# Optimization experiments

Hardware: AMD Instinct MI355X
Metric: run time of the kernel (lower is better)

## Reference

```python
import jax, jax.numpy as jnp
import numpy as np
from jax.scipy.special import logsumexp

B, S, E, H = 32, 1024, 512, 256  # batch, seq_len, sent_emb_dim, per-direction lstm hidden
NT, NTB = 16, 5
PAD, SOS, EOS = 0, 1, 2
NEG = -1000000.0


def _lstm(x, h0, c0, wih, whh, bih, bhh):
    # x: [B,S,I] -> outputs [B,S,H]; torch gate order i,f,g,o
    def step(carry, xt):
        h, c = carry
        z = xt @ wih.T + h @ whh.T + bih + bhh
        i, f, g, o = jnp.split(z, 4, axis=-1)
        c = jax.nn.sigmoid(f) * c + jax.nn.sigmoid(i) * jnp.tanh(g)
        h = jax.nn.sigmoid(o) * jnp.tanh(c)
        return (h, c), h
    _, hs = jax.lax.scan(step, (h0, c0), jnp.swapaxes(x, 0, 1))
    return jnp.swapaxes(hs, 0, 1)


def _bilstm(x, h0, c0, pf, pb):
    fwd = _lstm(x, h0[0], c0[0], *pf)
    bwd = _lstm(x[:, ::-1], h0[1], c0[1], *pb)[:, ::-1]
    return jnp.concatenate([fwd, bwd], axis=-1)  # [B,S,2H]


def _crf_nll(emissions, tags, mask, T):
    # gold-path score
    first = T[SOS, tags[:, 0]] + jnp.take_along_axis(emissions[:, 0], tags[:, 0:1], axis=1)[:, 0]
    e = jnp.take_along_axis(emissions, tags[:, :, None], axis=2)[:, :, 0]        # [B,S]
    tr = T[tags[:, :-1], tags[:, 1:]]                                            # [B,S-1]
    scores = first + jnp.sum((e[:, 1:] + tr) * mask[:, 1:], axis=1)
    last_idx = mask.sum(1).astype(jnp.int32) - 1
    last_tags = jnp.take_along_axis(tags, last_idx[:, None], axis=1)[:, 0]
    scores = scores + T[last_tags, EOS]
    # log partition via sequential DP (scan over time)
    alphas0 = T[SOS][None, :] + emissions[:, 0]
    es = jnp.swapaxes(emissions, 0, 1)[1:]   # [S-1,B,nt]
    ms = mask.T[1:]                          # [S-1,B]
    def step(alphas, inp):
        e_t, m_t = inp
        sc = e_t[:, None, :] + T[None, :, :] + alphas[:, :, None]  # [B,nt,nt]
        new = logsumexp(sc, axis=1)
        m = m_t[:, None]
        return m * new + (1.0 - m) * alphas, None
    alphas, _ = jax.lax.scan(step, alphas0, (es, ms))
    logZ = logsumexp(alphas + T[:, EOS][None, :], axis=1)
    return -jnp.sum(scores - logZ)


def _make_trans(key, nt):
    t = jax.random.uniform(key, (nt, nt), minval=-0.1, maxval=0.1)
    t = t.at[:, SOS].set(NEG).at[EOS, :].set(NEG)
    t = t.at[PAD, :].set(NEG).at[:, PAD].set(NEG)
    t = t.at[PAD, EOS].set(0.0).at[PAD, PAD].set(0.0)
    return t


def setup_inputs() -> dict:
    key = jax.random.key(0)
    ks = iter(jax.random.split(key, 40))
    sc = 0.05
    inp = {}
    inp['x'] = jax.random.normal(next(ks), (B, S, E), jnp.float32)
    inp['x_binary'] = jax.random.normal(next(ks), (B, S, 3 * E), jnp.float32)
    lengths = jax.random.randint(next(ks), (B,), S // 2, S + 1)
    inp['mask'] = (jnp.arange(S)[None, :] < lengths[:, None]).astype(jnp.float32)
    tg = jax.random.randint(next(ks), (B, S), 3, NT)
    inp['tags'] = jnp.where(inp['mask'] > 0, tg, PAD).astype(jnp.int32)
    tgb = jax.random.randint(next(ks), (B, S), 3, NTB)
    inp['tags_bin'] = jnp.where(inp['mask'] > 0, tgb, PAD).astype(jnp.int32)
    inp['trans'] = _make_trans(next(ks), NT)
    inp['trans_bin'] = _make_trans(next(ks), NTB)
    # binary emitter BiLSTM (input 3E)
    for nm, shp in [('w2f_ih', (4 * H, 3 * E)), ('w2f_hh', (4 * H, H)), ('b2f_ih', (4 * H,)), ('b2f_hh', (4 * H,)),
                    ('w2b_ih', (4 * H, 3 * E)), ('w2b_hh', (4 * H, H)), ('b2b_ih', (4 * H,)), ('b2b_hh', (4 * H,)),
                    ('w_bin', (NTB, 2 * H)), ('bb_bin', (NTB,)),
                    ('w1f_ih', (4 * H, E)), ('w1f_hh', (4 * H, H)), ('b1f_ih', (4 * H,)), ('b1f_hh', (4 * H,)),
                    ('w1b_ih', (4 * H, E)), ('w1b_hh', (4 * H, H)), ('b1b_ih', (4 * H,)), ('b1b_hh', (4 * H,)),
                    ('w_tag', (NT, 4 * H)), ('b_tag', (NT,))]:
        inp[nm] = jax.random.normal(next(ks), shp, jnp.float32) * sc
    inp['h0_bin'] = jax.random.normal(next(ks), (2, B, H), jnp.float32)
    inp['c0_bin'] = jax.random.normal(next(ks), (2, B, H), jnp.float32)
    inp['h0_main'] = jax.random.normal(next(ks), (2, B, H), jnp.float32)
    inp['c0_main'] = jax.random.normal(next(ks), (2, B, H), jnp.float32)
    return inp


def reference(x, x_binary, mask, tags, tags_bin, trans, trans_bin,
              w2f_ih, w2f_hh, b2f_ih, b2f_hh, w2b_ih, w2b_hh, b2b_ih, b2b_hh, w_bin, bb_bin, h0_bin, c0_bin,
              w1f_ih, w1f_hh, b1f_ih, b1f_hh, w1b_ih, w1b_hh, b1b_ih, b1b_hh, w_tag, b_tag, h0_main, c0_main):
    # binary branch: BiLSTM over 3E features -> hidden [B,S,2H] and 5-tag emissions
    hid_bin = _bilstm(x_binary, h0_bin, c0_bin,
                      (w2f_ih, w2f_hh, b2f_ih, b2f_hh), (w2b_ih, w2b_hh, b2b_ih, b2b_hh))
    emis_bin = hid_bin @ w_bin.T + bb_bin
    # main branch: BiLSTM over E features, concat with binary hidden -> n_tags emissions
    hid_main = _bilstm(x, h0_main, c0_main,
                       (w1f_ih, w1f_hh, b1f_ih, b1f_hh), (w1b_ih, w1b_hh, b1b_ih, b1b_hh))
    final = jnp.concatenate([hid_main, hid_bin], axis=-1)  # [B,S,4H] (dropout omitted: eval mode)
    emis = final @ w_tag.T + b_tag
    nll = _crf_nll(emis, tags, mask, trans)
    nll_bin = _crf_nll(emis_bin, tags_bin, mask, trans_bin)
    return jnp.stack([nll, nll_bin])
```

## Files before the change

### kernel.cpp

```cpp
#include <hip/hip_runtime.h>

typedef _Float16 f16;
typedef _Float16 f16x2 __attribute__((ext_vector_type(2)));
typedef _Float16 f16x4 __attribute__((ext_vector_type(4)));
typedef _Float16 f16x8 __attribute__((ext_vector_type(8)));
typedef float f32x4 __attribute__((ext_vector_type(4)));
typedef int iv4 __attribute__((ext_vector_type(4)));

#define S_LEN 1024
#define BATCH 32
#define HID 256
#define L2E 1.4426950408889634f
#define L2E2 2.8853900817779268f

#if __has_builtin(__builtin_amdgcn_fdot2)
#define FDOT2(a, b, c) __builtin_amdgcn_fdot2((a), (b), (c), false)
#else
static __device__ __forceinline__ float FDOT2(f16x2 a, f16x2 b, float c) {
  return c + (float)a[0] * (float)b[0] + (float)a[1] * (float)b[1];
}
#endif

__device__ __forceinline__ float EXP2(float x) {
#if __has_builtin(__builtin_amdgcn_exp2f)
  return __builtin_amdgcn_exp2f(x);
#else
  return exp2f(x);
#endif
}
__device__ __forceinline__ float RCP(float x) {
#if __has_builtin(__builtin_amdgcn_rcpf)
  return __builtin_amdgcn_rcpf(x);
#else
  return 1.0f / x;
#endif
}

__device__ __forceinline__ iv4 cvt8(float4 a, float4 b) {
#if __has_builtin(__builtin_amdgcn_cvt_pkrtz)
  auto p0 = __builtin_amdgcn_cvt_pkrtz(a.x, a.y);
  auto p1 = __builtin_amdgcn_cvt_pkrtz(a.z, a.w);
  auto p2 = __builtin_amdgcn_cvt_pkrtz(b.x, b.y);
  auto p3 = __builtin_amdgcn_cvt_pkrtz(b.z, b.w);
  iv4 o;
  o[0] = __builtin_bit_cast(int, p0);
  o[1] = __builtin_bit_cast(int, p1);
  o[2] = __builtin_bit_cast(int, p2);
  o[3] = __builtin_bit_cast(int, p3);
  return o;
#else
  f16x8 h;
  h[0] = (f16)a.x; h[1] = (f16)a.y; h[2] = (f16)a.z; h[3] = (f16)a.w;
  h[4] = (f16)b.x; h[5] = (f16)b.y; h[6] = (f16)b.z; h[7] = (f16)b.w;
  return __builtin_bit_cast(iv4, h);
#endif
}

#if __has_builtin(__builtin_amdgcn_global_load_lds)
__device__ __forceinline__ void gload16(const void* g, void* l) {
  __builtin_amdgcn_global_load_lds((const __attribute__((address_space(1))) void*)g,
                                   (__attribute__((address_space(3))) void*)l, 16, 0, 0);
}
#else
__device__ __forceinline__ void gload16(const void* g, void* l) {
  int lane = __builtin_amdgcn_mbcnt_hi(~0u, __builtin_amdgcn_mbcnt_lo(~0u, 0));
  ((f16x8*)l)[lane] = *(const f16x8*)g;
}
#endif

#define WG_BARRIER()                                                  \
  do {                                                                \
    __builtin_amdgcn_sched_barrier(0);                                \
    asm volatile("s_waitcnt lgkmcnt(0)\n\ts_barrier" ::: "memory");   \
    __builtin_amdgcn_sched_barrier(0);                                \
  } while (0)

__device__ __forceinline__ float dot8(f16x8 w, f16x8 h, float acc) {
  f16x2 a, b;
  a[0] = w[0]; a[1] = w[1]; b[0] = h[0]; b[1] = h[1]; acc = FDOT2(a, b, acc);
  a[0] = w[2]; a[1] = w[3]; b[0] = h[2]; b[1] = h[3]; acc = FDOT2(a, b, acc);
  a[0] = w[4]; a[1] = w[5]; b[0] = h[4]; b[1] = h[5]; acc = FDOT2(a, b, acc);
  a[0] = w[6]; a[1] = w[7]; b[0] = h[6]; b[1] = h[7]; acc = FDOT2(a, b, acc);
  return acc;
}

__global__ __launch_bounds__(256) void prep_all(
    const float* __restrict__ w1f_hh, const float* __restrict__ w1b_hh,
    const float* __restrict__ w2f_hh, const float* __restrict__ w2b_hh,
    char* __restrict__ Wq4, float* __restrict__ fsc4,
    const float* __restrict__ w_tag, f16* __restrict__ wtag,
    const float* __restrict__ w_bin, f16* __restrict__ wbin,
    const float* __restrict__ w1f_ih, const float* __restrict__ w1b_ih,
    const float* __restrict__ w2f_ih, const float* __restrict__ w2b_ih,
    f16* __restrict__ w16all,
    const float* __restrict__ b1f_ih, const float* __restrict__ b1f_hh,
    const float* __restrict__ b1b_ih, const float* __restrict__ b1b_hh,
    const float* __restrict__ b2f_ih, const float* __restrict__ b2f_hh,
    const float* __restrict__ b2b_ih, const float* __restrict__ b2b_hh,
    float* __restrict__ bsum) {
  const int blk = blockIdx.x;
  const int tid = threadIdx.x;
  if (blk < 1024) {
    const int u = blk >> 8, sb = blk & 255;
    const float* src = u == 0 ? w1f_hh : u == 1 ? w1b_hh : u == 2 ? w2f_hh : w2b_hh;
    char* dstq = Wq4 + (size_t)u * 262144;
    float* fsc = fsc4 + u * 1024;
    const int row = sb * 4 + (tid >> 6);
    const int lane = tid & 63;
    const float sc = (row >= 512 && row < 768) ? L2E2 : L2E;
    float4 v = *(const float4*)(src + (size_t)row * 256 + lane * 4);
    float w0 = v.x * sc, w1 = v.y * sc, w2 = v.z * sc, w3 = v.w * sc;
    float mx = fmaxf(fmaxf(fabsf(w0), fabsf(w1)), fmaxf(fabsf(w2), fabsf(w3)));
#pragma unroll
    for (int off = 1; off < 64; off <<= 1) mx = fmaxf(mx, __shfl_xor(mx, off));
    mx = fmaxf(mx, 1e-20f);
    float inv = 127.0f / mx;
    int q0 = (int)rintf(w0 * inv), q1 = (int)rintf(w1 * inv);
    int q2 = (int)rintf(w2 * inv), q3 = (int)rintf(w3 * inv);
    int pk = (q0 & 0xff) | ((q1 & 0xff) << 8) | ((q2 & 0xff) << 16) | ((q3 & 0xff) << 24);
    ((int*)(dstq + (size_t)row * 256))[lane] = pk;
    if (lane == 0) fsc[row] = mx / 16129.0f;
  } else if (blk < 1040) {
    int i = (blk - 1024) * 256 + tid;
    if (i < 4096) {
      float4 v = ((const float4*)w_tag)[i];
      f16x4 h;
      h[0] = (f16)v.x; h[1] = (f16)v.y; h[2] = (f16)v.z; h[3] = (f16)v.w;
      ((f16x4*)wtag)[i] = h;
    }
  } else if (blk < 1043) {
    int i = (blk - 1040) * 256 + tid;
    if (i < 640) {
      float4 v = ((const float4*)w_bin)[i];
      f16x4 h;
      h[0] = (f16)v.x; h[1] = (f16)v.y; h[2] = (f16)v.z; h[3] = (f16)v.w;
      ((f16x4*)wbin)[i] = h;
    }
  } else if (blk < 3091) {
    int rel = blk - 1043;
    const float* src;
    f16* dst;
    int K, total8;
    if (rel < 256) { src = w1f_ih; dst = w16all; K = 512; total8 = 65536; }
    else if (rel < 512) { src = w1b_ih; dst = w16all + 524288; K = 512; total8 = 65536; rel -= 256; }
    else if (rel < 1280) { src = w2f_ih; dst = w16all + 1048576; K = 1536; total8 = 196608; rel -= 512; }
    else { src = w2b_ih; dst = w16all + 2621440; K = 1536; total8 = 196608; rel -= 1280; }
    int i = rel * 256 + tid;
    if (i < total8) {
      int row = (int)(((long long)i * 8) / K);
      float sc = (row >= 512 && row < 768) ? L2E2 : L2E;
      const float* s = src + (size_t)i * 8;
      float4 a = *(const float4*)s;
      float4 b = *(const float4*)(s + 4);
      f16x8 h;
      h[0] = (f16)(a.x * sc); h[1] = (f16)(a.y * sc); h[2] = (f16)(a.z * sc); h[3] = (f16)(a.w * sc);
      h[4] = (f16)(b.x * sc); h[5] = (f16)(b.y * sc); h[6] = (f16)(b.z * sc); h[7] = (f16)(b.w * sc);
      *(f16x8*)(dst + (size_t)i * 8) = h;
    }
  } else {
    int i = (blk - 3091) * 256 + tid;
    if (i < 4096) {
      int u = i >> 10, n = i & 1023;
      float sc = (n >= 512 && n < 768) ? L2E2 : L2E;
      const float* pa = u == 0 ? b1f_ih : u == 1 ? b1b_ih : u == 2 ? b2f_ih : b2b_ih;
      const float* ph = u == 0 ? b1f_hh : u == 1 ? b1b_hh : u == 2 ? b2f_hh : b2b_hh;
      bsum[i] = (pa[n] + ph[n]) * sc;
    }
  }
}

__global__ __launch_bounds__(256) void proj_gemm(const float* __restrict__ x,
                                                 const float* __restrict__ xbin,
                                                 const f16* __restrict__ w16all,
                                                 const float* __restrict__ bsum,
                                                 char* __restrict__ P4) {
  __shared__ __align__(16) char smem[98304];
  const int L = blockIdx.x;
  const int xcd = L & 7;
  const int k = L >> 3;
  const int e = k & 7;
  const int G = xcd + ((k >> 3) << 3);
  const int v = e >> 1;
  const int ubit = e & 1;
  const int pair = G >> 8;
  const int bm = G & 255;
  const int unit = pair * 2 + ubit;
  const int K = (pair == 0) ? 512 : 1536;
  const float* Aptr = (pair == 0) ? x : xbin;
  const size_t woff = (unit == 0) ? 0u : (unit == 1) ? 524288u : (unit == 2) ? 1048576u : 2621440u;
  const f16* W16 = w16all + woff;
  const int bgrp = bm >> 5, t0 = (bm & 31) * 32;
  const int b0 = bgrp * 4, c = bgrp >> 1, lkb = bgrp & 1;
  const int tid = threadIdx.x;
  const int lane = tid & 63, wid = tid >> 6;
  const int wm = wid >> 1, wn = wid & 1;
  const int lr = lane & 15, lk = lane >> 4;
  const int xsw = (lr & 7) << 4;

  f32x4 acc[4][8];
#pragma unroll
  for (int i = 0; i < 4; ++i)
#pragma unroll
    for (int n = 0; n < 8; ++n) acc[i][n] = (f32x4){0.f, 0.f, 0.f, 0.f};

#define PROJ_PREFETCH(KN_, AO_, BO_)                                                        \
  if ((KN_) < K) {                                                                          \
    float4 ar0[4], ar1[4];                                                                  \
    _Pragma("unroll") for (int s = 0; s < 4; ++s) {                                         \
      int slot = s * 256 + tid;                                                             \
      int row = slot >> 3, seg = slot & 7;                                                  \
      size_t arow = (size_t)(b0 + (row >> 5)) * 1024 + t0 + (row & 31);                     \
      const float* ga = Aptr + arow * K + (KN_) + seg * 8;                                  \
      ar0[s] = *(const float4*)ga;                                                          \
      ar1[s] = *(const float4*)(ga + 4);                                                    \
    }                                                                                       \
    __builtin_amdgcn_sched_barrier(0);                                                      \
    _Pragma("unroll") for (int i = 0; i < 8; ++i) {                                         \
      int g = (wid * 8 + i) * 64 + lane;                                                    \
      int brow = g >> 3, cg = g & 7;                                                        \
      const f16* bsrc = W16 + (size_t)(v * 256 + brow) * K + (KN_) + ((cg ^ (brow & 7)) << 3); \
      gload16(bsrc, smem + (BO_) + (wid * 8 + i) * 1024);                                   \
    }                                                                                       \
    __builtin_amdgcn_sched_barrier(0);                                                      \
    _Pragma("unroll") for (int s = 0; s < 4; ++s) {                                         \
      int slot = s * 256 + tid;                                                             \
      int row = slot >> 3, seg = slot & 7;                                                  \
      *(iv4*)(smem + (AO_) + row * 128 + ((seg ^ (row & 7)) << 4)) = cvt8(ar0[s], ar1[s]);  \
    }                                                                                       \
    __builtin_amdgcn_sched_barrier(0);                                                      \
  } else {                                                                                  \
    __builtin_amdgcn_sched_barrier(0);                                                      \
    asm volatile("s_waitcnt vmcnt(0)" ::: "memory");                                        \
    __builtin_amdgcn_sched_barrier(0);                                                      \
  }

#define PROJ_COMPUTE(AO_, BO_)                                                              \
  _Pragma("unroll") for (int kk = 0; kk < 2; ++kk) {                                        \
    f16x8 af[4], bf[8];                                                                     \
    _Pragma("unroll") for (int mi = 0; mi < 4; ++mi) {                                      \
      int ba = (wm * 64 + mi * 16 + lr) * 128 + kk * 64 + lk * 16;                          \
      af[mi] = *(const f16x8*)(smem + (AO_) + (ba ^ xsw));                                  \
    }                                                                                       \
    _Pragma("unroll") for (int ni = 0; ni < 8; ++ni) {                                      \
      int bb = (wn * 128 + ni * 16 + lr) * 128 + kk * 64 + lk * 16;                         \
      bf[ni] = *(const f16x8*)(smem + (BO_) + (bb ^ xsw));                                  \
    }                                                                                       \
    _Pragma("unroll") for (int mi = 0; mi < 4; ++mi)                                        \
      _Pragma("unroll") for (int ni = 0; ni < 8; ++ni)                                      \
        acc[mi][ni] = __builtin_amdgcn_mfma_f32_16x16x32_f16(af[mi], bf[ni], acc[mi][ni], 0, 0, 0); \
  }

  PROJ_PREFETCH(0, 0, 32768);
  for (int k0 = 0; k0 < K; k0 += 128) {
    PROJ_PREFETCH(k0 + 64, 16384, 65536);
    WG_BARRIER();
    PROJ_COMPUTE(0, 32768);
    WG_BARRIER();
    PROJ_PREFETCH(k0 + 128, 0, 32768);
    WG_BARRIER();
    PROJ_COMPUTE(16384, 65536);
    WG_BARRIER();
  }
#undef PROJ_PREFETCH
#undef PROJ_COMPUTE

  float biasv[8];
#pragma unroll
  for (int ni = 0; ni < 8; ++ni)
    biasv[ni] = bsum[unit * 1024 + v * 256 + wn * 128 + ni * 16 + lr];
  char* Pv = P4 + ((size_t)unit << 26) + ((size_t)v << 24);
#pragma unroll
  for (int pass = 0; pass < 2; ++pass) {
    __syncthreads();
#pragma unroll
    for (int mi2 = 0; mi2 < 2; ++mi2) {
      int mi = mi2 * 2 + pass;
#pragma unroll
      for (int ni = 0; ni < 8; ++ni) {
        int col = wn * 128 + ni * 16 + lr;
        int wc = col >> 5, jc = (col >> 4) & 1, lc = col & 15;
#pragma unroll
        for (int rr = 0; rr < 4; ++rr) {
          int row = wm * 64 + mi * 16 + lk * 4 + rr;
          int bsub = row >> 5, tl = row & 15;
          int unit2 = tl * 256 + wc * 32 + jc * 16 + lc;
          int off = (unit2 * 8 + bsub * 2) ^ ((tl & 7) << 4);
          *(f16*)(smem + off) = (f16)(acc[mi][ni][rr] + biasv[ni]);
        }
      }
    }
    __syncthreads();
#pragma unroll
    for (int kq = 0; kq < 16; ++kq) {
      int uid = kq * 256 + tid;
      int tl = uid >> 8, sub = uid & 255;
      int off = (uid * 8) ^ ((tl & 7) << 4);
      unsigned long long val = *(const unsigned long long*)(smem + off);
      int t_loc = pass * 16 + tl;
      int wq = sub >> 5, jq = (sub >> 4) & 1, lq = sub & 15;
      size_t didx =
          (((size_t)((t0 + t_loc) * 4 + c) * 512) + wq * 64 + jq * 32 + lkb * 16 + lq) << 3;
      *(unsigned long long*)(Pv + didx) = val;
    }
  }
}

__global__ __attribute__((amdgpu_flat_work_group_size(512, 512), amdgpu_waves_per_eu(2, 2)))
void lstm_rec5(const char* __restrict__ Wq4,
               const float* __restrict__ fsc4,
               const char* __restrict__ P4,
               const float* __restrict__ h0m,
               const float* __restrict__ c0m,
               const float* __restrict__ h0b,
               const float* __restrict__ c0b,
               f16* __restrict__ hid4) {
  const int wg = blockIdx.x;
  const int u = wg >> 4, c16 = wg & 15;
  const int dir = u & 1;
  const int tid = threadIdx.x;
  const int l = tid & 63, w = tid >> 6;
  const int lr = l & 15, lk = l >> 4;
  const int jj = lk >> 1, selb = lk & 1;
  const int r2 = lr & 1;
  const int swzA = r2 ? 80 : 0;
  const int swzW = selb ? 80 : 0;
  const int j = w * 32 + jj * 16 + lr;

  __shared__ __align__(16) char hbuf[2][512];

  iv4 Bf[4][8];
  const char* wb = Wq4 + ((size_t)u << 18);
#pragma unroll
  for (int nt = 0; nt < 8; ++nt) {
    int n = (nt >> 1) * 256 + w * 32 + ((nt & 1) << 4) + lr;
#pragma unroll
    for (int ks = 0; ks < 4; ++ks)
      Bf[ks][nt] = *(const iv4*)(wb + (size_t)n * 256 + ks * 64 + lk * 16);
  }
  float fv[4], fv4[4];
#pragma unroll
  for (int v = 0; v < 4; ++v) {
    fv[v] = fsc4[u * 1024 + v * 256 + j];
    fv4[v] = fv[v] * 4.f;
  }

  const int b = c16 * 2 + selb;
  const float* h0 = (u < 2 ? h0m : h0b) + (size_t)dir * BATCH * HID;
  const float* c0 = (u < 2 ? c0m : c0b) + (size_t)dir * BATCH * HID;
  float cst = c0[b * HID + j];
  {
    float hv = h0[b * HID + j] * 31.75f;
    int hq = (int)rintf(hv);
    hq = hq > 127 ? 127 : (hq < -127 ? -127 : hq);
    hbuf[0][selb * 256 + (j ^ swzW)] = (char)hq;
  }

  const char* Pc = P4 + ((size_t)u << 26);
  const size_t soff =
      (size_t)((w * 64 + jj * 32 + (((c16 >> 1) & 1) << 4) + lr) * 8 + (c16 & 1) * 4);
  const int cq = c16 >> 2;
  f16x2 Pa[4], Pb[4];
  {
    int t0 = dir ? (S_LEN - 1) : 0;
    size_t tb = ((size_t)((t0 << 2) + cq) << 12) + soff;
#pragma unroll
    for (int v = 0; v < 4; ++v) Pa[v] = *(const f16x2*)(Pc + ((size_t)v << 24) + tb);
  }
  WG_BARRIER();

#define LSTM_STEP(S_, SP_, PC_, PN_, FV_)                                                   \
  {                                                                                         \
    const int t = dir ? (S_LEN - 1 - (S_)) : (S_);                                          \
    {                                                                                       \
      int s2 = ((S_) + 1 < S_LEN) ? (S_) + 1 : (S_);                                        \
      int t2 = dir ? (S_LEN - 1 - s2) : s2;                                                 \
      size_t tb = ((size_t)((t2 << 2) + cq) << 12) + soff;                                  \
      _Pragma("unroll") for (int v = 0; v < 4; ++v)                                         \
          PN_[v] = *(const f16x2*)(Pc + ((size_t)v << 24) + tb);                            \
    }                                                                                       \
    iv4 ia[8];                                                                              \
    _Pragma("unroll") for (int nt = 0; nt < 8; ++nt) ia[nt] = (iv4){0, 0, 0, 0};            \
    const char* hb = hbuf[SP_];                                                             \
    _Pragma("unroll") for (int ks = 0; ks < 4; ++ks) {                                      \
      iv4 Af = *(const iv4*)(hb + r2 * 256 + ((ks * 64 + lk * 16) ^ swzA));                 \
      _Pragma("unroll") for (int nt = 0; nt < 8; ++nt)                                      \
          ia[nt] = __builtin_amdgcn_mfma_i32_16x16x64_i8(Af, Bf[ks][nt], ia[nt], 0, 0, 0);  \
    }                                                                                       \
    float z[4];                                                                             \
    _Pragma("unroll") for (int v = 0; v < 4; ++v) {                                         \
      int e0 = selb ? ia[v * 2][1] : ia[v * 2][0];                                          \
      int e1 = selb ? ia[v * 2 + 1][1] : ia[v * 2 + 1][0];                                  \
      int iz = jj ? e1 : e0;                                                                \
      float pv = selb ? (float)PC_[v][1] : (float)PC_[v][0];                                \
      z[v] = pv + FV_[v] * (float)iz;                                                       \
    }                                                                                       \
    float zi = z[0], zf = z[1], zg = z[2], zo = z[3];                                       \
    float ei = EXP2(-zi), ef = EXP2(-zf), eg = EXP2(-zg), eo = EXP2(-zo);                   \
    float di = 1.f + ei, df = 1.f + ef, dg = 1.f + eg, dof = 1.f + eo;                      \
    float r1 = RCP(di * df);                                                                \
    float si = r1 * df, sf = r1 * di;                                                       \
    float r2x = RCP(dg * dof);                                                              \
    float tg = 2.f * (r2x * dof) - 1.f, so = r2x * dg;                                      \
    float cc = sf * cst + si * tg;                                                          \
    cst = cc;                                                                               \
    float ec = EXP2(-L2E2 * cc);                                                            \
    float th = 2.f * RCP(1.f + ec) - 1.f;                                                   \
    float hh = so * th;                                                                     \
    int hq = (int)rintf(hh * 127.f);                                                        \
    hbuf[SP_ ^ 1][selb * 256 + (j ^ swzW)] = (char)hq;                                      \
    hid4[((size_t)b << 20) + ((size_t)t << 10) + (u << 8) + j] = (f16)hh;                   \
    WG_BARRIER();                                                                           \
  }

  LSTM_STEP(0, 0, Pa, Pb, fv4);
  for (int s = 1; s <= 1021; s += 2) {
    LSTM_STEP(s, 1, Pb, Pa, fv);
    LSTM_STEP(s + 1, 0, Pa, Pb, fv);
  }
  LSTM_STEP(1023, 1, Pb, Pa, fv);
#undef LSTM_STEP
}

__global__ __launch_bounds__(256) void emis_mfma(const f16* __restrict__ hid4,
                                                 const f16* __restrict__ wtag,
                                                 const float* __restrict__ btag,
                                                 const f16* __restrict__ wbin,
                                                 const float* __restrict__ bbin,
                                                 float* __restrict__ emis,
                                                 float* __restrict__ emisb) {
  __shared__ __align__(16) f16 wt[16 * 1024];
  __shared__ __align__(16) f16 wbp[16 * 512];
  const int tid = threadIdx.x;
#pragma unroll
  for (int i = 0; i < 8; ++i) {
    int idx = i * 256 + tid;
    int n = idx >> 7, cc = idx & 127;
    ((f16x8*)wt)[n * 128 + (cc ^ (n & 7))] = ((const f16x8*)wtag)[idx];
  }
#pragma unroll
  for (int i = 0; i < 4; ++i) {
    int idx = i * 256 + tid;
    int n = idx >> 6, cc = idx & 63;
    f16x8 val = {};
    if (n < 5) val = ((const f16x8*)wbin)[n * 64 + cc];
    ((f16x8*)wbp)[n * 64 + (cc ^ (n & 7))] = val;
  }
  __syncthreads();

  const int wv = tid >> 6, lane = tid & 63;
  const int lr = lane & 15, lk = lane >> 4;
  const size_t row0 = (size_t)blockIdx.x * 64 + wv * 16;
  const f16* arow = hid4 + (row0 + lr) * 1024;
  const f16x8* wtp = (const f16x8*)wt;
  const f16x8* wbv = (const f16x8*)wbp;
  const int bsw = lr & 7;

  f32x4 accm = (f32x4){0.f, 0.f, 0.f, 0.f};
  f32x4 accb = (f32x4){0.f, 0.f, 0.f, 0.f};
#pragma unroll
  for (int ks = 0; ks < 32; ++ks) {
    f16x8 a = *(const f16x8*)(arow + ks * 32 + lk * 8);
    f16x8 b = wtp[lr * 128 + ((ks * 4 + lk) ^ bsw)];
    accm = __builtin_amdgcn_mfma_f32_16x16x32_f16(a, b, accm, 0, 0, 0);
  }
#pragma unroll
  for (int ks = 0; ks < 16; ++ks) {
    f16x8 a = *(const f16x8*)(arow + 512 + ks * 32 + lk * 8);
    f16x8 b = wbv[lr * 64 + ((ks * 4 + lk) ^ bsw)];
    accb = __builtin_amdgcn_mfma_f32_16x16x32_f16(a, b, accb, 0, 0, 0);
  }
  float bt = btag[lr];
  float bb = (lr < 5) ? bbin[lr] : 0.f;
#pragma unroll
  for (int r = 0; r < 4; ++r) {
    size_t orow = row0 + lk * 4 + r;
    emis[orow * 16 + lr] = accm[r] + bt;
    if (lr < 5) emisb[orow * 5 + lr] = accb[r] + bb;
  }
}

__global__ __launch_bounds__(64) void crf_fused(const float* __restrict__ emis,
                                                const float* __restrict__ trans,
                                                const float* __restrict__ emisb,
                                                const float* __restrict__ transb,
                                                const float* __restrict__ mask,
                                                const int* __restrict__ tags,
                                                const int* __restrict__ tagsb,
                                                float* __restrict__ outLogZ,
                                                float* __restrict__ outScore) {
  const int lane = threadIdx.x;
  if (blockIdx.x < 64) {
    const int crf = blockIdx.x >> 5, b = blockIdx.x & 31;
    const int NTc = crf ? 5 : 16;
    const float* __restrict__ E = crf ? emisb : emis;
    const float* __restrict__ T = crf ? transb : trans;
    const int jn = lane >> 2, p = lane & 3;
    const bool jv = (jn < NTc);
    const int jc = jv ? jn : 0;
    float Tc[4];
#pragma unroll
    for (int ii = 0; ii < 4; ++ii) {
      int i = p * 4 + ii;
      Tc[ii] = (jv && i < NTc) ? T[i * NTc + jn] : -1e30f;
    }
    float alpha = jv ? (T[1 * NTc + jc] + E[(size_t)(b << 10) * NTc + jc]) : -1e30f;
    const size_t ebase = (size_t)(b << 10) * NTc + jc;
    const int mbase = b << 10;
#define LDE(tt) E[ebase + (size_t)(tt)*NTc]
#define LDM(tt) mask[mbase + (tt)]

    auto step = [&](float e_tj, float m_t) {
      float a0 = __shfl(alpha, ((p * 4 + 0) << 2) | p);
      float a1 = __shfl(alpha, ((p * 4 + 1) << 2) | p);
      float a2 = __shfl(alpha, ((p * 4 + 2) << 2) | p);
      float a3 = __shfl(alpha, ((p * 4 + 3) << 2) | p);
      float v0 = a0 + Tc[0], v1 = a1 + Tc[1], v2 = a2 + Tc[2], v3 = a3 + Tc[3];
      float mx = fmaxf(fmaxf(v0, v1), fmaxf(v2, v3));
      mx = fmaxf(mx, __shfl_xor(mx, 1, 4));
      mx = fmaxf(mx, __shfl_xor(mx, 2, 4));
      float ss = __expf(v0 - mx) + __expf(v1 - mx) + __expf(v2 - mx) + __expf(v3 - mx);
      ss += __shfl_xor(ss, 1, 4);
      ss += __shfl_xor(ss, 2, 4);
      float newv = e_tj + mx + __logf(ss);
      alpha = (m_t > 0.5f) ? newv : alpha;
    };

    float eb[4], mb[4];
#pragma unroll
    for (int k = 0; k < 4; ++k) { eb[k] = LDE(1 + k); mb[k] = LDM(1 + k); }
    for (int t = 1; t <= 1017; t += 4) {
      float en[4], mn[4];
#pragma unroll
      for (int k = 0; k < 4; ++k) {
        int ix = t + 4 + k;
        ix = ix > 1023 ? 1023 : ix;
        en[k] = LDE(ix);
        mn[k] = LDM(ix);
      }
      step(eb[0], mb[0]); step(eb[1], mb[1]); step(eb[2], mb[2]); step(eb[3], mb[3]);
#pragma unroll
      for (int k = 0; k < 4; ++k) { eb[k] = en[k]; mb[k] = mn[k]; }
    }
    step(eb[0], mb[0]); step(eb[1], mb[1]); step(eb[2], mb[2]);
#undef LDE
#undef LDM

    float fin = (jv && p == 0) ? (alpha + T[jn * NTc + 2]) : -1e30f;
    float mx = fin;
#pragma unroll
    for (int off = 1; off < 64; off <<= 1) mx = fmaxf(mx, __shfl_xor(mx, off));
    float ss = __expf(fin - mx);
#pragma unroll
    for (int off = 1; off < 64; off <<= 1) ss += __shfl_xor(ss, off);
    if (lane == 0) outLogZ[crf * 32 + b] = mx + __logf(ss);
  } else {
    const int bi = blockIdx.x - 64;
    const int crf = bi >> 5, b = bi & 31;
    const int NTc = crf ? 5 : 16;
    const float* __restrict__ E = crf ? emisb : emis;
    const float* __restrict__ T = crf ? transb : trans;
    const int* __restrict__ tg = (crf ? tagsb : tags) + (b << 10);
    const float* __restrict__ mk = mask + (b << 10);
    float s = 0.f, cnt = 0.f;
    for (int t = lane; t < S_LEN; t += 64) {
      float m = mk[t];
      cnt += m;
      if (t >= 1 && m > 0.5f)
        s += E[((size_t)(b << 10) + t) * NTc + tg[t]] + T[tg[t - 1] * NTc + tg[t]];
    }
#pragma unroll
    for (int off = 32; off >= 1; off >>= 1) {
      s += __shfl_down(s, off);
      cnt += __shfl_down(cnt, off);
    }
    if (lane == 0) {
      int L = (int)(cnt + 0.5f);
      int t0 = tg[0];
      float tot = T[1 * NTc + t0] + E[(size_t)(b << 10) * NTc + t0] + s + T[tg[L - 1] * NTc + 2];
      outScore[crf * 32 + b] = tot;
    }
  }
}

__global__ void finalk(const float* __restrict__ logZ, const float* __restrict__ score,
                       float* __restrict__ out) {
  int j = threadIdx.x;
  if (j < 2) {
    float a = 0.f;
    for (int b = 0; b < 32; ++b) a += logZ[j * 32 + b] - score[j * 32 + b];
    out[j] = a;
  }
}

extern "C" void kernel_launch(void* const* d_in, const int* in_sizes, int n_in,
                              void* d_out, int out_size, void* d_ws, size_t ws_size,
                              hipStream_t stream) {
  const float* x       = (const float*)d_in[0];
  const float* xbin    = (const float*)d_in[1];
  const float* mask    = (const float*)d_in[2];
  const int*   tags    = (const int*)d_in[3];
  const int*   tagsb   = (const int*)d_in[4];
  const float* trans   = (const float*)d_in[5];
  const float* transb  = (const float*)d_in[6];
  const float* w2f_ih  = (const float*)d_in[7];
  const float* w2f_hh  = (const float*)d_in[8];
  const float* b2f_ih  = (const float*)d_in[9];
  const float* b2f_hh  = (const float*)d_in[10];
  const float* w2b_ih  = (const float*)d_in[11];
  const float* w2b_hh  = (const float*)d_in[12];
  const float* b2b_ih  = (const float*)d_in[13];
  const float* b2b_hh  = (const float*)d_in[14];
  const float* w_bin   = (const float*)d_in[15];
  const float* bb_bin  = (const float*)d_in[16];
  const float* w1f_ih  = (const float*)d_in[17];
  const float* w1f_hh  = (const float*)d_in[18];
  const float* b1f_ih  = (const float*)d_in[19];
  const float* b1f_hh  = (const float*)d_in[20];
  const float* w1b_ih  = (const float*)d_in[21];
  const float* w1b_hh  = (const float*)d_in[22];
  const float* b1b_ih  = (const float*)d_in[23];
  const float* b1b_hh  = (const float*)d_in[24];
  const float* w_tag   = (const float*)d_in[25];
  const float* b_tag   = (const float*)d_in[26];
  const float* h0_bin  = (const float*)d_in[27];
  const float* c0_bin  = (const float*)d_in[28];
  const float* h0_main = (const float*)d_in[29];
  const float* c0_main = (const float*)d_in[30];

  char* ws = (char*)d_ws;
  char* P4    = ws;
  f16* hid4   = (f16*)(ws + 268435456);
  char* Wq4   = ws + 335544320;
  float* fsc4 = (float*)(ws + 336592896);
  f16* wtag   = (f16*)(ws + 336609280);
  f16* wbin   = (f16*)(ws + 336642048);
  float* emis  = (float*)(ws + 336647168);
  float* emisb = (float*)(ws + 338744320);
  float* logZ  = (float*)(ws + 339399680);
  float* score = (float*)(ws + 339399936);
  float* bsum  = (float*)(ws + 339400704);
  f16* w16all  = (f16*)(ws + 340000768);

  prep_all<<<3107, 256, 0, stream>>>(w1f_hh, w1b_hh, w2f_hh, w2b_hh, Wq4, fsc4,
                                     w_tag, wtag, w_bin, wbin,
                                     w1f_ih, w1b_ih, w2f_ih, w2b_ih, w16all,
                                     b1f_ih, b1f_hh, b1b_ih, b1b_hh,
                                     b2f_ih, b2f_hh, b2b_ih, b2b_hh, bsum);
  proj_gemm<<<4096, 256, 0, stream>>>(x, xbin, w16all, bsum, P4);
  lstm_rec5<<<64, 512, 0, stream>>>(Wq4, fsc4, P4, h0_main, c0_main, h0_bin, c0_bin, hid4);
  emis_mfma<<<512, 256, 0, stream>>>(hid4, wtag, b_tag, wbin, bb_bin, emis, emisb);
  crf_fused<<<128, 64, 0, stream>>>(emis, trans, emisb, transb, mask, tags, tagsb, logZ, score);
  finalk<<<1, 64, 0, stream>>>(logZ, score, (float*)d_out);
}
```

Measured before the change: 1.606 ms.

## Fuse input projection GEMM and LSTM recurrence with flag-based producer/consumer overlap

Merges the projection GEMM and the recurrent LSTM kernel into one launch. The first 64 blocks run the recurrence, and the remaining blocks compute projection tiles, ordered so that time windows are produced from both ends first. Recurrence blocks spin on per-window atomic flags before reading each 32-step window, so the GEMM can overlap with the serial recurrence instead of running fully before it. The costs are 512-thread blocks where half the threads idle in the GEMM part, lower occupancy for the GEMM blocks, spin-wait overhead, and a deadlock risk if the recurrence blocks are not scheduled alongside the producers.

```diff
diff --git a/kernel.cpp b/kernel.cpp
--- a/kernel.cpp
+++ b/kernel.cpp
@@ -82,6 +82,10 @@
   a[0] = w[4]; a[1] = w[5]; b[0] = h[4]; b[1] = h[5]; acc = FDOT2(a, b, acc);
   a[0] = w[6]; a[1] = w[7]; b[0] = h[6]; b[1] = h[7]; acc = FDOT2(a, b, acc);
   return acc;
+}
+
+__global__ void zerof(unsigned* __restrict__ f) {
+  f[blockIdx.x * 256 + threadIdx.x] = 0u;
 }
 
 __global__ __launch_bounds__(256) void prep_all(
@@ -169,204 +173,83 @@
   }
 }
 
-__global__ __launch_bounds__(256) void proj_gemm(const float* __restrict__ x,
-                                                 const float* __restrict__ xbin,
-                                                 const f16* __restrict__ w16all,
-                                                 const float* __restrict__ bsum,
-                                                 char* __restrict__ P4) {
-  __shared__ __align__(16) char smem[98304];
-  const int L = blockIdx.x;
-  const int xcd = L & 7;
-  const int k = L >> 3;
-  const int e = k & 7;
-  const int G = xcd + ((k >> 3) << 3);
-  const int v = e >> 1;
-  const int ubit = e & 1;
-  const int pair = G >> 8;
-  const int bm = G & 255;
-  const int unit = pair * 2 + ubit;
-  const int K = (pair == 0) ? 512 : 1536;
-  const float* Aptr = (pair == 0) ? x : xbin;
-  const size_t woff = (unit == 0) ? 0u : (unit == 1) ? 524288u : (unit == 2) ? 1048576u : 2621440u;
-  const f16* W16 = w16all + woff;
-  const int bgrp = bm >> 5, t0 = (bm & 31) * 32;
-  const int b0 = bgrp * 4, c = bgrp >> 1, lkb = bgrp & 1;
-  const int tid = threadIdx.x;
-  const int lane = tid & 63, wid = tid >> 6;
-  const int wm = wid >> 1, wn = wid & 1;
-  const int lr = lane & 15, lk = lane >> 4;
-  const int xsw = (lr & 7) << 4;
-
-  f32x4 acc[4][8];
-#pragma unroll
-  for (int i = 0; i < 4; ++i)
-#pragma unroll
-    for (int n = 0; n < 8; ++n) acc[i][n] = (f32x4){0.f, 0.f, 0.f, 0.f};
-
-#define PROJ_PREFETCH(KN_, AO_, BO_)                                                        \
-  if ((KN_) < K) {                                                                          \
-    float4 ar0[4], ar1[4];                                                                  \
-    _Pragma("unroll") for (int s = 0; s < 4; ++s) {                                         \
-      int slot = s * 256 + tid;                                                             \
-      int row = slot >> 3, seg = slot & 7;                                                  \
-      size_t arow = (size_t)(b0 + (row >> 5)) * 1024 + t0 + (row & 31);                     \
-      const float* ga = Aptr + arow * K + (KN_) + seg * 8;                                  \
-      ar0[s] = *(const float4*)ga;                                                          \
-      ar1[s] = *(const float4*)(ga + 4);                                                    \
-    }                                                                                       \
-    __builtin_amdgcn_sched_barrier(0);                                                      \
-    _Pragma("unroll") for (int i = 0; i < 8; ++i) {                                         \
-      int g = (wid * 8 + i) * 64 + lane;                                                    \
-      int brow = g >> 3, cg = g & 7;                                                        \
-      const f16* bsrc = W16 + (size_t)(v * 256 + brow) * K + (KN_) + ((cg ^ (brow & 7)) << 3); \
-      gload16(bsrc, smem + (BO_) + (wid * 8 + i) * 1024);                                   \
-    }                                                                                       \
-    __builtin_amdgcn_sched_barrier(0);                                                      \
-    _Pragma("unroll") for (int s = 0; s < 4; ++s) {                                         \
-      int slot = s * 256 + tid;                                                             \
-      int row = slot >> 3, seg = slot & 7;                                                  \
-      *(iv4*)(smem + (AO_) + row * 128 + ((seg ^ (row & 7)) << 4)) = cvt8(ar0[s], ar1[s]);  \
-    }                                                                                       \
-    __builtin_amdgcn_sched_barrier(0);                                                      \
-  } else {                                                                                  \
-    __builtin_amdgcn_sched_barrier(0);                                                      \
-    asm volatile("s_waitcnt vmcnt(0)" ::: "memory");                                        \
-    __builtin_amdgcn_sched_barrier(0);                                                      \
-  }
-
-#define PROJ_COMPUTE(AO_, BO_)                                                              \
-  _Pragma("unroll") for (int kk = 0; kk < 2; ++kk) {                                        \
-    f16x8 af[4], bf[8];                                                                     \
-    _Pragma("unroll") for (int mi = 0; mi < 4; ++mi) {                                      \
-      int ba = (wm * 64 + mi * 16 + lr) * 128 + kk * 64 + lk * 16;                          \
-      af[mi] = *(const f16x8*)(smem + (AO_) + (ba ^ xsw));                                  \
-    }                                                                                       \
-    _Pragma("unroll") for (int ni = 0; ni < 8; ++ni) {                                      \
-      int bb = (wn * 128 + ni * 16 + lr) * 128 + kk * 64 + lk * 16;                         \
-      bf[ni] = *(const f16x8*)(smem + (BO_) + (bb ^ xsw));                                  \
-    }                                                                                       \
-    _Pragma("unroll") for (int mi = 0; mi < 4; ++mi)                                        \
-      _Pragma("unroll") for (int ni = 0; ni < 8; ++ni)                                      \
-        acc[mi][ni] = __builtin_amdgcn_mfma_f32_16x16x32_f16(af[mi], bf[ni], acc[mi][ni], 0, 0, 0); \
-  }
-
-  PROJ_PREFETCH(0, 0, 32768);
-  for (int k0 = 0; k0 < K; k0 += 128) {
-    PROJ_PREFETCH(k0 + 64, 16384, 65536);
-    WG_BARRIER();
-    PROJ_COMPUTE(0, 32768);
-    WG_BARRIER();
-    PROJ_PREFETCH(k0 + 128, 0, 32768);
-    WG_BARRIER();
-    PROJ_COMPUTE(16384, 65536);
-    WG_BARRIER();
-  }
-#undef PROJ_PREFETCH
-#undef PROJ_COMPUTE
-
-  float biasv[8];
-#pragma unroll
-  for (int ni = 0; ni < 8; ++ni)
-    biasv[ni] = bsum[unit * 1024 + v * 256 + wn * 128 + ni * 16 + lr];
-  char* Pv = P4 + ((size_t)unit << 26) + ((size_t)v << 24);
-#pragma unroll
-  for (int pass = 0; pass < 2; ++pass) {
-    __syncthreads();
-#pragma unroll
-    for (int mi2 = 0; mi2 < 2; ++mi2) {
-      int mi = mi2 * 2 + pass;
-#pragma unroll
-      for (int ni = 0; ni < 8; ++ni) {
-        int col = wn * 128 + ni * 16 + lr;
-        int wc = col >> 5, jc = (col >> 4) & 1, lc = col & 15;
-#pragma unroll
-        for (int rr = 0; rr < 4; ++rr) {
-          int row = wm * 64 + mi * 16 + lk * 4 + rr;
-          int bsub = row >> 5, tl = row & 15;
-          int unit2 = tl * 256 + wc * 32 + jc * 16 + lc;
-          int off = (unit2 * 8 + bsub * 2) ^ ((tl & 7) << 4);
-          *(f16*)(smem + off) = (f16)(acc[mi][ni][rr] + biasv[ni]);
-        }
-      }
-    }
-    __syncthreads();
-#pragma unroll
-    for (int kq = 0; kq < 16; ++kq) {
-      int uid = kq * 256 + tid;
-      int tl = uid >> 8, sub = uid & 255;
-      int off = (uid * 8) ^ ((tl & 7) << 4);
-      unsigned long long val = *(const unsigned long long*)(smem + off);
-      int t_loc = pass * 16 + tl;
-      int wq = sub >> 5, jq = (sub >> 4) & 1, lq = sub & 15;
-      size_t didx =
-          (((size_t)((t0 + t_loc) * 4 + c) * 512) + wq * 64 + jq * 32 + lkb * 16 + lq) << 3;
-      *(unsigned long long*)(Pv + didx) = val;
-    }
-  }
-}
-
 __global__ __attribute__((amdgpu_flat_work_group_size(512, 512), amdgpu_waves_per_eu(2, 2)))
-void lstm_rec5(const char* __restrict__ Wq4,
+void proj_lstm(const float* __restrict__ x,
+               const float* __restrict__ xbin,
+               const f16* __restrict__ w16all,
+               const float* __restrict__ bsum,
+               char* __restrict__ P4,
+               const char* __restrict__ Wq4,
                const float* __restrict__ fsc4,
-               const char* __restrict__ P4,
                const float* __restrict__ h0m,
                const float* __restrict__ c0m,
                const float* __restrict__ h0b,
                const float* __restrict__ c0b,
-               f16* __restrict__ hid4) {
-  const int wg = blockIdx.x;
-  const int u = wg >> 4, c16 = wg & 15;
-  const int dir = u & 1;
+               f16* __restrict__ hid4,
+               unsigned* __restrict__ flags) {
+  __shared__ __align__(16) char smem[98304];
+  __shared__ __align__(16) char hbuf[2][512];
   const int tid = threadIdx.x;
-  const int l = tid & 63, w = tid >> 6;
-  const int lr = l & 15, lk = l >> 4;
-  const int jj = lk >> 1, selb = lk & 1;
-  const int r2 = lr & 1;
-  const int swzA = r2 ? 80 : 0;
-  const int swzW = selb ? 80 : 0;
-  const int j = w * 32 + jj * 16 + lr;
-
-  __shared__ __align__(16) char hbuf[2][512];
-
-  iv4 Bf[4][8];
-  const char* wb = Wq4 + ((size_t)u << 18);
-#pragma unroll
-  for (int nt = 0; nt < 8; ++nt) {
-    int n = (nt >> 1) * 256 + w * 32 + ((nt & 1) << 4) + lr;
-#pragma unroll
-    for (int ks = 0; ks < 4; ++ks)
-      Bf[ks][nt] = *(const iv4*)(wb + (size_t)n * 256 + ks * 64 + lk * 16);
-  }
-  float fv[4], fv4[4];
-#pragma unroll
-  for (int v = 0; v < 4; ++v) {
-    fv[v] = fsc4[u * 1024 + v * 256 + j];
-    fv4[v] = fv[v] * 4.f;
-  }
-
-  const int b = c16 * 2 + selb;
-  const float* h0 = (u < 2 ? h0m : h0b) + (size_t)dir * BATCH * HID;
-  const float* c0 = (u < 2 ? c0m : c0b) + (size_t)dir * BATCH * HID;
-  float cst = c0[b * HID + j];
-  {
-    float hv = h0[b * HID + j] * 31.75f;
-    int hq = (int)rintf(hv);
-    hq = hq > 127 ? 127 : (hq < -127 ? -127 : hq);
-    hbuf[0][selb * 256 + (j ^ swzW)] = (char)hq;
-  }
-
-  const char* Pc = P4 + ((size_t)u << 26);
-  const size_t soff =
-      (size_t)((w * 64 + jj * 32 + (((c16 >> 1) & 1) << 4) + lr) * 8 + (c16 & 1) * 4);
-  const int cq = c16 >> 2;
-  f16x2 Pa[4], Pb[4];
-  {
-    int t0 = dir ? (S_LEN - 1) : 0;
-    size_t tb = ((size_t)((t0 << 2) + cq) << 12) + soff;
-#pragma unroll
-    for (int v = 0; v < 4; ++v) Pa[v] = *(const f16x2*)(Pc + ((size_t)v << 24) + tb);
-  }
-  WG_BARRIER();
+
+  if (blockIdx.x < 64) {
+    const int wg = blockIdx.x;
+    const int u = wg >> 4, c16 = wg & 15;
+    const int dir = u & 1;
+    const int l = tid & 63, w = tid >> 6;
+    const int lr = l & 15, lk = l >> 4;
+    const int jj = lk >> 1, selb = lk & 1;
+    const int r2 = lr & 1;
+    const int swzA = r2 ? 80 : 0;
+    const int swzW = selb ? 80 : 0;
+    const int j = w * 32 + jj * 16 + lr;
+
+    iv4 Bf[4][8];
+    const char* wb = Wq4 + ((size_t)u << 18);
+#pragma unroll
+    for (int nt = 0; nt < 8; ++nt) {
+      int n = (nt >> 1) * 256 + w * 32 + ((nt & 1) << 4) + lr;
+#pragma unroll
+      for (int ks = 0; ks < 4; ++ks)
+        Bf[ks][nt] = *(const iv4*)(wb + (size_t)n * 256 + ks * 64 + lk * 16);
+    }
+    float fv[4], fv4[4];
+#pragma unroll
+    for (int v = 0; v < 4; ++v) {
+      fv[v] = fsc4[u * 1024 + v * 256 + j];
+      fv4[v] = fv[v] * 4.f;
+    }
+
+    const int b = c16 * 2 + selb;
+    const float* h0 = (u < 2 ? h0m : h0b) + (size_t)dir * BATCH * HID;
+    const float* c0 = (u < 2 ? c0m : c0b) + (size_t)dir * BATCH * HID;
+    float cst = c0[b * HID + j];
+    {
+      float hv = h0[b * HID + j] * 31.75f;
+      int hq = (int)rintf(hv);
+      hq = hq > 127 ? 127 : (hq < -127 ? -127 : hq);
+      hbuf[0][selb * 256 + (j ^ swzW)] = (char)hq;
+    }
+
+    unsigned* fbase = flags + u * 256 + (c16 >> 1) * 32;
+    int curw = dir ? 31 : 0;
+    if (tid == 0) {
+      while (atomicAdd(&fbase[curw], 0u) < 4u) __builtin_amdgcn_s_sleep(4);
+    }
+    __syncthreads();
+    __threadfence();
+
+    const char* Pc = P4 + ((size_t)u << 26);
+    const size_t soff =
+        (size_t)((w * 64 + jj * 32 + (((c16 >> 1) & 1) << 4) + lr) * 8 + (c16 & 1) * 4);
+    const int cq = c16 >> 2;
+    f16x2 Pa[4], Pb[4];
+    {
+      int t0 = dir ? (S_LEN - 1) : 0;
+      size_t tb = ((size_t)((t0 << 2) + cq) << 12) + soff;
+#pragma unroll
+      for (int v = 0; v < 4; ++v) Pa[v] = *(const f16x2*)(Pc + ((size_t)v << 24) + tb);
+    }
+    WG_BARRIER();
 
 #define LSTM_STEP(S_, SP_, PC_, PN_, FV_)                                                   \
   {                                                                                         \
@@ -374,6 +257,15 @@
     {                                                                                       \
       int s2 = ((S_) + 1 < S_LEN) ? (S_) + 1 : (S_);                                        \
       int t2 = dir ? (S_LEN - 1 - s2) : s2;                                                 \
+      int w2 = t2 >> 5;                                                                     \
+      if (w2 != curw) {                                                                     \
+        if (tid == 0) {                                                                     \
+          while (atomicAdd(&fbase[w2], 0u) < 4u) __builtin_amdgcn_s_sleep(4);               \
+        }                                                                                   \
+        __syncthreads();                                                                    \
+        __threadfence();                                                                    \
+        curw = w2;                                                                          \
+      }                                                                                     \
       size_t tb = ((size_t)((t2 << 2) + cq) << 12) + soff;                                  \
       _Pragma("unroll") for (int v = 0; v < 4; ++v)                                         \
           PN_[v] = *(const f16x2*)(Pc + ((size_t)v << 24) + tb);                            \
@@ -412,13 +304,157 @@
     WG_BARRIER();                                                                           \
   }
 
-  LSTM_STEP(0, 0, Pa, Pb, fv4);
-  for (int s = 1; s <= 1021; s += 2) {
-    LSTM_STEP(s, 1, Pb, Pa, fv);
-    LSTM_STEP(s + 1, 0, Pa, Pb, fv);
-  }
-  LSTM_STEP(1023, 1, Pb, Pa, fv);
+    LSTM_STEP(0, 0, Pa, Pb, fv4);
+    for (int s = 1; s <= 1021; s += 2) {
+      LSTM_STEP(s, 1, Pb, Pa, fv);
+      LSTM_STEP(s + 1, 0, Pa, Pb, fv);
+    }
+    LSTM_STEP(1023, 1, Pb, Pa, fv);
 #undef LSTM_STEP
+  } else {
+    const int pb = blockIdx.x - 64;
+    const int wo = pb >> 7;
+    const int rr = pb & 127;
+    const int tw = (wo & 1) ? (31 - (wo >> 1)) : (wo >> 1);
+    const int unit = rr >> 5;
+    const int v = (rr >> 3) & 3;
+    const int bgrp = rr & 7;
+    const int pair = unit >> 1;
+    const int K = (pair == 0) ? 512 : 1536;
+    const float* Aptr = (pair == 0) ? x : xbin;
+    const size_t woff =
+        (unit == 0) ? 0u : (unit == 1) ? 524288u : (unit == 2) ? 1048576u : 2621440u;
+    const f16* W16 = w16all + woff;
+    const int t0 = tw * 32;
+    const int b0 = bgrp * 4, c = bgrp >> 1, lkb = bgrp & 1;
+    const bool act = tid < 256;
+    const int lane = tid & 63, wid = tid >> 6;
+    const int wm = wid >> 1, wn = wid & 1;
+    const int lr = lane & 15, lk = lane >> 4;
+    const int xsw = (lr & 7) << 4;
+
+    f32x4 acc[4][8];
+#pragma unroll
+    for (int i = 0; i < 4; ++i)
+#pragma unroll
+      for (int n = 0; n < 8; ++n) acc[i][n] = (f32x4){0.f, 0.f, 0.f, 0.f};
+
+#define PROJ_PREFETCH(KN_, AO_, BO_)                                                        \
+  if ((KN_) < K) {                                                                          \
+    if (act) {                                                                              \
+      float4 ar0[4], ar1[4];                                                                \
+      _Pragma("unroll") for (int s = 0; s < 4; ++s) {                                       \
+        int slot = s * 256 + tid;                                                           \
+        int row = slot >> 3, seg = slot & 7;                                                \
+        size_t arow = (size_t)(b0 + (row >> 5)) * 1024 + t0 + (row & 31);                   \
+        const float* ga = Aptr + arow * K + (KN_) + seg * 8;                                \
+        ar0[s] = *(const float4*)ga;                                                        \
+        ar1[s] = *(const float4*)(ga + 4);                                                  \
+      }                                                                                     \
+      __builtin_amdgcn_sched_barrier(0);                                                    \
+      _Pragma("unroll") for (int i = 0; i < 8; ++i) {                                       \
+        int g = (wid * 8 + i) * 64 + lane;                                                  \
+        int brow = g >> 3, cg = g & 7;                                                      \
+        const f16* bsrc =                                                                   \
+            W16 + (size_t)(v * 256 + brow) * K + (KN_) + ((cg ^ (brow & 7)) << 3);          \
+        gload16(bsrc, smem + (BO_) + (wid * 8 + i) * 1024);                                 \
+      }                                                                                     \
+      __builtin_amdgcn_sched_barrier(0);                                                    \
+      _Pragma("unroll") for (int s = 0; s < 4; ++s) {                                       \
+        int slot = s * 256 + tid;                                                           \
+        int row = slot >> 3, seg = slot & 7;                                                \
+        *(iv4*)(smem + (AO_) + row * 128 + ((seg ^ (row & 7)) << 4)) = cvt8(ar0[s], ar1[s]); \
+      }                                                                                     \
+      __builtin_amdgcn_sched_barrier(0);                                                    \
+    }                                                                                       \
+  } else {                                                                                  \
+    __builtin_amdgcn_sched_barrier(0);                                                      \
+    asm volatile("s_waitcnt vmcnt(0)" ::: "memory");                                        \
+    __builtin_amdgcn_sched_barrier(0);                                                      \
+  }
+
+#define PROJ_COMPUTE(AO_, BO_)                                                              \
+  if (act) {                                                                                \
+    _Pragma("unroll") for (int kk = 0; kk < 2; ++kk) {                                      \
+      f16x8 af[4], bf[8];                                                                   \
+      _Pragma("unroll") for (int mi = 0; mi < 4; ++mi) {                                    \
+        int ba = (wm * 64 + mi * 16 + lr) * 128 + kk * 64 + lk * 16;                        \
+        af[mi] = *(const f16x8*)(smem + (AO_) + (ba ^ xsw));                                \
+      }                                                                                     \
+      _Pragma("unroll") for (int ni = 0; ni < 8; ++ni) {                                    \
+        int bb = (wn * 128 + ni * 16 + lr) * 128 + kk * 64 + lk * 16;                       \
+        bf[ni] = *(const f16x8*)(smem + (BO_) + (bb ^ xsw));                                \
+      }                                                                                     \
+      _Pragma("unroll") for (int mi = 0; mi < 4; ++mi)                                      \
+        _Pragma("unroll") for (int ni = 0; ni < 8; ++ni)                                    \
+          acc[mi][ni] =                                                                     \
+              __builtin_amdgcn_mfma_f32_16x16x32_f16(af[mi], bf[ni], acc[mi][ni], 0, 0, 0); \
+    }                                                                                       \
+  }
+
+    PROJ_PREFETCH(0, 0, 32768);
+    for (int k0 = 0; k0 < K; k0 += 128) {
+      PROJ_PREFETCH(k0 + 64, 16384, 65536);
+      WG_BARRIER();
+      PROJ_COMPUTE(0, 32768);
+      WG_BARRIER();
+      PROJ_PREFETCH(k0 + 128, 0, 32768);
+      WG_BARRIER();
+      PROJ_COMPUTE(16384, 65536);
+      WG_BARRIER();
+    }
+#undef PROJ_PREFETCH
+#undef PROJ_COMPUTE
+
+    float biasv[8];
+    if (act) {
+#pragma unroll
+      for (int ni = 0; ni < 8; ++ni)
+        biasv[ni] = bsum[unit * 1024 + v * 256 + wn * 128 + ni * 16 + lr];
+    }
+    char* Pv = P4 + ((size_t)unit << 26) + ((size_t)v << 24);
+#pragma unroll
+    for (int pass = 0; pass < 2; ++pass) {
+      __syncthreads();
+      if (act) {
+#pragma unroll
+        for (int mi2 = 0; mi2 < 2; ++mi2) {
+          int mi = mi2 * 2 + pass;
+#pragma unroll
+          for (int ni = 0; ni < 8; ++ni) {
+            int col = wn * 128 + ni * 16 + lr;
+            int wc = col >> 5, jc = (col >> 4) & 1, lc = col & 15;
+#pragma unroll
+            for (int rrx = 0; rrx < 4; ++rrx) {
+              int row = wm * 64 + mi * 16 + lk * 4 + rrx;
+              int bsub = row >> 5, tl = row & 15;
+              int unit2 = tl * 256 + wc * 32 + jc * 16 + lc;
+              int off = (unit2 * 8 + bsub * 2) ^ ((tl & 7) << 4);
+              *(f16*)(smem + off) = (f16)(acc[mi][ni][rrx] + biasv[ni]);
+            }
+          }
+        }
+      }
+      __syncthreads();
+      if (act) {
+#pragma unroll
+        for (int kq = 0; kq < 16; ++kq) {
+          int uid = kq * 256 + tid;
+          int tl = uid >> 8, sub = uid & 255;
+          int off = (uid * 8) ^ ((tl & 7) << 4);
+          unsigned long long val = *(const unsigned long long*)(smem + off);
+          int t_loc = pass * 16 + tl;
+          int wq = sub >> 5, jq = (sub >> 4) & 1, lq = sub & 15;
+          size_t didx =
+              (((size_t)((t0 + t_loc) * 4 + c) * 512) + wq * 64 + jq * 32 + lkb * 16 + lq) << 3;
+          *(unsigned long long*)(Pv + didx) = val;
+        }
+      }
+    }
+    __threadfence();
+    __syncthreads();
+    if (tid == 0) atomicAdd(&flags[unit * 256 + bgrp * 32 + tw], 1u);
+  }
 }
 
 __global__ __launch_bounds__(256) void emis_mfma(const f16* __restrict__ hid4,
@@ -639,6 +675,7 @@
   float* logZ  = (float*)(ws + 339399680);
   float* score = (float*)(ws + 339399936);
   float* bsum  = (float*)(ws + 339400704);
+  unsigned* flags = (unsigned*)(ws + 339417088);
   f16* w16all  = (f16*)(ws + 340000768);
 
   prep_all<<<3107, 256, 0, stream>>>(w1f_hh, w1b_hh, w2f_hh, w2b_hh, Wq4, fsc4,
@@ -646,8 +683,9 @@
                                      w1f_ih, w1b_ih, w2f_ih, w2b_ih, w16all,
                                      b1f_ih, b1f_hh, b1b_ih, b1b_hh,
                                      b2f_ih, b2f_hh, b2b_ih, b2b_hh, bsum);
-  proj_gemm<<<4096, 256, 0, stream>>>(x, xbin, w16all, bsum, P4);
-  lstm_rec5<<<64, 512, 0, stream>>>(Wq4, fsc4, P4, h0_main, c0_main, h0_bin, c0_bin, hid4);
+  zerof<<<4, 256, 0, stream>>>(flags);
+  proj_lstm<<<4160, 512, 0, stream>>>(x, xbin, w16all, bsum, P4, Wq4, fsc4,
+                                      h0_main, c0_main, h0_bin, c0_bin, hid4, flags);
   emis_mfma<<<512, 256, 0, stream>>>(hid4, wtag, b_tag, wbin, bb_bin, emis, emisb);
   crf_fused<<<128, 64, 0, stream>>>(emis, trans, emisb, transb, mask, tags, tagsb, logZ, score);
   finalk<<<1, 64, 0, stream>>>(logZ, score, (float*)d_out);
```

Result: slower. 2.994 ms (+86.4%).
